# Performance work log

Hardware: AMD Instinct MI355X
Metric: run time of the kernel (lower is better)

## Reference

```python
import jax, jax.numpy as jnp
import numpy as np


def setup_inputs() -> dict:
    key = jax.random.key(0)
    k1, _ = jax.random.split(key)
    N, C, T, F = 32, 128, 512, 32
    x = jax.random.normal(k1, (N, C, T, F), dtype=jnp.float32)
    sigma = jnp.ones((1,), dtype=jnp.float32)
    return {"x": x, "sigma": sigma}


def reference(x, sigma):
    # x: (N, C, T, F); pairwise squared L2 distance between the C channels
    # over the T axis, independently per (batch, filter) pair.
    N, C, T, F = x.shape
    xr = jnp.transpose(x, (0, 3, 1, 2)).reshape(N * F, C, T)  # (N*F, C, T)
    # ||a-b||^2 = ||a||^2 + ||b||^2 - 2 a.b  (GEMM-based cdist)
    sq = jnp.sum(xr * xr, axis=-1)                 # (N*F, C)
    gram = jnp.einsum('bct,bdt->bcd', xr, xr)      # (N*F, C, C)
    d2 = sq[:, :, None] + sq[:, None, :] - 2.0 * gram
    d2 = jnp.maximum(d2, 0.0)                      # guard tiny negatives
    sig = jnp.reshape(sigma, ())
    kern = jnp.exp(-d2 / (2.0 * sig * sig))        # (N*F, C, C)
    kern = kern.reshape(N, F, C, C)
    return jnp.transpose(kern, (0, 2, 3, 1))       # (N, C, C, F)
```

## Files before the change

### kernel.cpp

```cpp
#include <hip/hip_runtime.h>

typedef __attribute__((ext_vector_type(4))) float f32x4;
typedef __attribute__((ext_vector_type(8))) __bf16 bf16x8;
typedef __attribute__((address_space(1))) unsigned int gu32;
typedef __attribute__((address_space(3))) unsigned int lu32;

#define PN 32
#define PC 128
#define PT 512
#define PF 32

__device__ inline unsigned short f2bf(float x) {
  unsigned int u = __float_as_uint(x);
  return (unsigned short)((u + 0x7FFFu + ((u >> 16) & 1u)) >> 16);
}

__global__ __launch_bounds__(256) void pack_kernel(const float* __restrict__ x,
                                                   unsigned short* __restrict__ xt) {
  const int nc = blockIdx.x;
  const int n = nc >> 7, c = nc & 127;
  const float4* src4 = (const float4*)(x + (size_t)nc * (PT * PF));
  __shared__ unsigned short lds[32][522];
  const int tid = threadIdx.x;

  #pragma unroll
  for (int i = 0; i < 16; ++i) {
    int idx = i * 256 + tid;
    float4 v = src4[idx];
    int flat = idx << 2;
    int t = flat >> 5, f0 = flat & 31;
    lds[f0 + 0][t] = f2bf(v.x);
    lds[f0 + 1][t] = f2bf(v.y);
    lds[f0 + 2][t] = f2bf(v.z);
    lds[f0 + 3][t] = f2bf(v.w);
  }
  __syncthreads();

  #pragma unroll
  for (int i = 0; i < 16; ++i) {
    int idx = i * 256 + tid;
    int f = idx >> 7;
    int t4 = (idx & 127) << 2;
    ushort4 v;
    v.x = lds[f][t4 + 0];
    v.y = lds[f][t4 + 1];
    v.z = lds[f][t4 + 2];
    v.w = lds[f][t4 + 3];
    ushort4* dst = (ushort4*)(xt + (((size_t)(n * PF + f) * PC + c) * PT));
    dst[idx & 127] = v;
  }
}

template <bool COAL>
__global__ __launch_bounds__(256) void gram_kernel(const unsigned short* __restrict__ xt,
                                                   const float* __restrict__ sigma,
                                                   float* __restrict__ dst) {
  const int b = blockIdx.x;
  const int n = b >> 5, f = b & 31;
  const unsigned short* A = xt + (size_t)b * PC * PT;

  __shared__ __align__(16) unsigned short lds[PC * 64];
  __shared__ float sq[PC];

  const int tid = threadIdx.x;
  const int wv = tid >> 6, ln = tid & 63;
  const int r0 = (wv >> 1) * 64, c0 = (wv & 1) * 64;
  const int lr = ln & 15, lq = ln >> 4;

  f32x4 acc[4][4];
  #pragma unroll
  for (int m = 0; m < 4; ++m)
    #pragma unroll
    for (int nn = 0; nn < 4; ++nn)
      acc[m][nn] = (f32x4){0.f, 0.f, 0.f, 0.f};

  const int srow = ln >> 3;
  const int sblk = (ln & 7) ^ srow;

  for (int ks = 0; ks < 8; ++ks) {
    const int t0 = ks * 64;
    #pragma unroll
    for (int i = 0; i < 4; ++i) {
      int slot = i * 4 + wv;
      int crow = slot * 8 + srow;
      const unsigned short* g = A + (size_t)crow * PT + t0 + sblk * 8;
      __builtin_amdgcn_global_load_lds((gu32*)g, (lu32*)(&lds[slot * 512]), 16, 0, 0);
    }
    __syncthreads();

    #pragma unroll
    for (int kk = 0; kk < 64; kk += 32) {
      bf16x8 av[4], bv[4];
      #pragma unroll
      for (int m = 0; m < 4; ++m) {
        int row = r0 + m * 16 + lr;
        av[m] = *(const bf16x8*)((const char*)lds + row * 128 +
                                 ((((kk >> 3) + lq) ^ (row & 7)) << 4));
      }
      #pragma unroll
      for (int m = 0; m < 4; ++m) {
        int row = c0 + m * 16 + lr;
        bv[m] = *(const bf16x8*)((const char*)lds + row * 128 +
                                 ((((kk >> 3) + lq) ^ (row & 7)) << 4));
      }
      #pragma unroll
      for (int m = 0; m < 4; ++m)
        #pragma unroll
        for (int nn = 0; nn < 4; ++nn)
          acc[m][nn] = __builtin_amdgcn_mfma_f32_16x16x32_bf16(av[m], bv[nn], acc[m][nn], 0, 0, 0);
    }
    __syncthreads();
  }

  #pragma unroll
  for (int m = 0; m < 4; ++m) {
    int rowb = r0 + m * 16 + lq * 4;
    int col  = c0 + m * 16 + lr;
    #pragma unroll
    for (int j = 0; j < 4; ++j)
      if (rowb + j == col) sq[col] = acc[m][m][j];
  }
  __syncthreads();

  const float sg = sigma[0];
  const float inv = 0.5f / (sg * sg);
  #pragma unroll
  for (int m = 0; m < 4; ++m) {
    #pragma unroll
    for (int nn = 0; nn < 4; ++nn) {
      int col = c0 + nn * 16 + lr;
      #pragma unroll
      for (int j = 0; j < 4; ++j) {
        int row = r0 + m * 16 + lq * 4 + j;
        float g = acc[m][nn][j];
        float d2 = fmaxf(sq[row] + sq[col] - 2.0f * g, 0.0f);
        float v = __expf(-d2 * inv);
        if (COAL) {
          dst[(size_t)b * (PC * PC) + row * PC + col] = v;
        } else {
          dst[(size_t)n * (PC * PC * PF) + ((size_t)row * PC + col) * PF + f] = v;
        }
      }
    }
  }
}

__global__ __launch_bounds__(256) void unpermute_kernel(const float* __restrict__ tmp,
                                                        float* __restrict__ out) {
  const int blk = blockIdx.x;
  const int n = blk >> 7, i = blk & 127;
  __shared__ float lds[PF][PC + 1];
  const int tid = threadIdx.x;

  const float* src = tmp + (size_t)n * PF * PC * PC + (size_t)i * PC;
  #pragma unroll
  for (int it = 0; it < 16; ++it) {
    int idx = it * 256 + tid;
    int fr = idx >> 7, j = idx & 127;
    lds[fr][j] = src[(size_t)fr * (PC * PC) + j];
  }
  __syncthreads();

  float4* dst4 = (float4*)(out + ((size_t)(n * PC) + i) * (PC * PF));
  #pragma unroll
  for (int it = 0; it < 4; ++it) {
    int idx4 = it * 256 + tid;
    int j = idx4 >> 3, f0 = (idx4 & 7) << 2;
    float4 v;
    v.x = lds[f0 + 0][j];
    v.y = lds[f0 + 1][j];
    v.z = lds[f0 + 2][j];
    v.w = lds[f0 + 3][j];
    dst4[idx4] = v;
  }
}

extern "C" void kernel_launch(void* const* d_in, const int* in_sizes, int n_in,
                              void* d_out, int out_size, void* d_ws, size_t ws_size,
                              hipStream_t stream) {
  const float* x = (const float*)d_in[0];
  const float* sigma = (const float*)d_in[1];
  float* out = (float*)d_out;

  unsigned short* xt = (unsigned short*)d_ws;
  const size_t xt_bytes = (size_t)PN * PF * PC * PT * 2;
  const size_t tmp_bytes = (size_t)PN * PF * PC * PC * 4;
  const bool coal = ws_size >= xt_bytes + tmp_bytes;

  hipLaunchKernelGGL(pack_kernel, dim3(PN * PC), dim3(256), 0, stream, x, xt);
  if (coal) {
    float* tmp = (float*)((char*)d_ws + xt_bytes);
    hipLaunchKernelGGL((gram_kernel<true>), dim3(PN * PF), dim3(256), 0, stream, xt, sigma, tmp);
    hipLaunchKernelGGL(unpermute_kernel, dim3(PN * PC), dim3(256), 0, stream, tmp, out);
  } else {
    hipLaunchKernelGGL((gram_kernel<false>), dim3(PN * PF), dim3(256), 0, stream, xt, sigma, out);
  }
}
```

Before: 444.9 us.

## Double-buffer LDS tiles in gram kernel and store intermediate kernel matrix as bf16

```diff
diff --git a/kernel.cpp b/kernel.cpp
--- a/kernel.cpp
+++ b/kernel.cpp
@@ -13,6 +13,9 @@
 __device__ inline unsigned short f2bf(float x) {
   unsigned int u = __float_as_uint(x);
   return (unsigned short)((u + 0x7FFFu + ((u >> 16) & 1u)) >> 16);
+}
+__device__ inline float bf2f(unsigned short b) {
+  return __uint_as_float(((unsigned int)b) << 16);
 }
 
 __global__ __launch_bounds__(256) void pack_kernel(const float* __restrict__ x,
@@ -54,12 +57,12 @@
 template <bool COAL>
 __global__ __launch_bounds__(256) void gram_kernel(const unsigned short* __restrict__ xt,
                                                    const float* __restrict__ sigma,
-                                                   float* __restrict__ dst) {
+                                                   void* __restrict__ dstv) {
   const int b = blockIdx.x;
   const int n = b >> 5, f = b & 31;
   const unsigned short* A = xt + (size_t)b * PC * PT;
 
-  __shared__ __align__(16) unsigned short lds[PC * 64];
+  __shared__ __align__(16) unsigned short lds[2][PC * 64];
   __shared__ float sq[PC];
 
   const int tid = threadIdx.x;
@@ -77,30 +80,40 @@
   const int srow = ln >> 3;
   const int sblk = (ln & 7) ^ srow;
 
+  #pragma unroll
+  for (int i = 0; i < 4; ++i) {
+    int slot = i * 4 + wv;
+    int crow = slot * 8 + srow;
+    const unsigned short* g = A + (size_t)crow * PT + 0 + sblk * 8;
+    __builtin_amdgcn_global_load_lds((gu32*)g, (lu32*)(&lds[0][slot * 512]), 16, 0, 0);
+  }
+  __syncthreads();
+
   for (int ks = 0; ks < 8; ++ks) {
-    const int t0 = ks * 64;
-    #pragma unroll
-    for (int i = 0; i < 4; ++i) {
-      int slot = i * 4 + wv;
-      int crow = slot * 8 + srow;
-      const unsigned short* g = A + (size_t)crow * PT + t0 + sblk * 8;
-      __builtin_amdgcn_global_load_lds((gu32*)g, (lu32*)(&lds[slot * 512]), 16, 0, 0);
+    if (ks < 7) {
+      const int t1 = (ks + 1) * 64;
+      #pragma unroll
+      for (int i = 0; i < 4; ++i) {
+        int slot = i * 4 + wv;
+        int crow = slot * 8 + srow;
+        const unsigned short* g = A + (size_t)crow * PT + t1 + sblk * 8;
+        __builtin_amdgcn_global_load_lds((gu32*)g, (lu32*)(&lds[(ks + 1) & 1][slot * 512]), 16, 0, 0);
+      }
     }
-    __syncthreads();
-
+    const unsigned short* L = lds[ks & 1];
     #pragma unroll
     for (int kk = 0; kk < 64; kk += 32) {
       bf16x8 av[4], bv[4];
       #pragma unroll
       for (int m = 0; m < 4; ++m) {
         int row = r0 + m * 16 + lr;
-        av[m] = *(const bf16x8*)((const char*)lds + row * 128 +
+        av[m] = *(const bf16x8*)((const char*)L + row * 128 +
                                  ((((kk >> 3) + lq) ^ (row & 7)) << 4));
       }
       #pragma unroll
       for (int m = 0; m < 4; ++m) {
         int row = c0 + m * 16 + lr;
-        bv[m] = *(const bf16x8*)((const char*)lds + row * 128 +
+        bv[m] = *(const bf16x8*)((const char*)L + row * 128 +
                                  ((((kk >> 3) + lq) ^ (row & 7)) << 4));
       }
       #pragma unroll
@@ -136,28 +149,32 @@
         float d2 = fmaxf(sq[row] + sq[col] - 2.0f * g, 0.0f);
         float v = __expf(-d2 * inv);
         if (COAL) {
-          dst[(size_t)b * (PC * PC) + row * PC + col] = v;
+          ((unsigned short*)dstv)[(size_t)b * (PC * PC) + row * PC + col] = f2bf(v);
         } else {
-          dst[(size_t)n * (PC * PC * PF) + ((size_t)row * PC + col) * PF + f] = v;
+          ((float*)dstv)[(size_t)n * (PC * PC * PF) + ((size_t)row * PC + col) * PF + f] = v;
         }
       }
     }
   }
 }
 
-__global__ __launch_bounds__(256) void unpermute_kernel(const float* __restrict__ tmp,
+__global__ __launch_bounds__(256) void unpermute_kernel(const unsigned short* __restrict__ tmp,
                                                         float* __restrict__ out) {
   const int blk = blockIdx.x;
   const int n = blk >> 7, i = blk & 127;
   __shared__ float lds[PF][PC + 1];
   const int tid = threadIdx.x;
 
-  const float* src = tmp + (size_t)n * PF * PC * PC + (size_t)i * PC;
-  #pragma unroll
-  for (int it = 0; it < 16; ++it) {
-    int idx = it * 256 + tid;
-    int fr = idx >> 7, j = idx & 127;
-    lds[fr][j] = src[(size_t)fr * (PC * PC) + j];
+  const unsigned short* src = tmp + (size_t)n * PF * PC * PC + (size_t)i * PC;
+  #pragma unroll
+  for (int it = 0; it < 4; ++it) {
+    int idx4 = it * 256 + tid;
+    int fr = idx4 >> 5, j4 = (idx4 & 31) << 2;
+    ushort4 v = *(const ushort4*)(src + (size_t)fr * (PC * PC) + j4);
+    lds[fr][j4 + 0] = bf2f(v.x);
+    lds[fr][j4 + 1] = bf2f(v.y);
+    lds[fr][j4 + 2] = bf2f(v.z);
+    lds[fr][j4 + 3] = bf2f(v.w);
   }
   __syncthreads();
 
@@ -184,15 +201,15 @@
 
   unsigned short* xt = (unsigned short*)d_ws;
   const size_t xt_bytes = (size_t)PN * PF * PC * PT * 2;
-  const size_t tmp_bytes = (size_t)PN * PF * PC * PC * 4;
+  const size_t tmp_bytes = (size_t)PN * PF * PC * PC * 2;
   const bool coal = ws_size >= xt_bytes + tmp_bytes;
 
   hipLaunchKernelGGL(pack_kernel, dim3(PN * PC), dim3(256), 0, stream, x, xt);
   if (coal) {
-    float* tmp = (float*)((char*)d_ws + xt_bytes);
-    hipLaunchKernelGGL((gram_kernel<true>), dim3(PN * PF), dim3(256), 0, stream, xt, sigma, tmp);
+    unsigned short* tmp = (unsigned short*)((char*)d_ws + xt_bytes);
+    hipLaunchKernelGGL((gram_kernel<true>), dim3(PN * PF), dim3(256), 0, stream, xt, sigma, (void*)tmp);
     hipLaunchKernelGGL(unpermute_kernel, dim3(PN * PC), dim3(256), 0, stream, tmp, out);
   } else {
-    hipLaunchKernelGGL((gram_kernel<false>), dim3(PN * PF), dim3(256), 0, stream, xt, sigma, out);
-  }
-}
+    hipLaunchKernelGGL((gram_kernel<false>), dim3(PN * PF), dim3(256), 0, stream, xt, sigma, (void*)out);
+  }
+}
```

Measured after the change: 433.4 us. 1.03x faster.
